# Kernel tuning notes

Hardware: AMD Instinct MI355X
Metric: run time of the kernel (lower is better)

The kernel has to match this reference:

```python
import jax, jax.numpy as jnp
import numpy as np

N_NODES = 50000
BN_EPS = 1e-5


def setup_inputs() -> dict:
    key = jax.random.key(0)
    ks = jax.random.split(key, 6)
    N, E, CIN, CH, COUT = N_NODES, 800000, 128, 256, 128
    node_feat = jax.random.normal(ks[0], (N, CIN), dtype=jnp.float32)
    edge_index = jax.random.randint(ks[1], (2, E), 0, N, dtype=jnp.int64)
    # Glorot-ish init for weights
    W1 = jax.random.normal(ks[2], (CIN, CH), dtype=jnp.float32) / np.sqrt(CIN)
    b1 = jnp.zeros((CH,), dtype=jnp.float32)
    bn_gamma = jnp.ones((CH,), dtype=jnp.float32)
    bn_beta = jnp.zeros((CH,), dtype=jnp.float32)
    W2 = jax.random.normal(ks[3], (CH, COUT), dtype=jnp.float32) / np.sqrt(CH)
    b2 = jnp.zeros((COUT,), dtype=jnp.float32)
    return {"node_feat": node_feat, "edge_index": edge_index, "W1": W1, "b1": b1,
            "bn_gamma": bn_gamma, "bn_beta": bn_beta, "W2": W2, "b2": b2}


def gcn_conv(x, W, b, src, dst, n_nodes):
    """PyG GCNConv: out = D^-1/2 (A+I) D^-1/2 (x W) + b."""
    h = x @ W                                   # [N, C_out]
    loop = jnp.arange(n_nodes, dtype=src.dtype)
    src_f = jnp.concatenate([src, loop])        # self-loops appended
    dst_f = jnp.concatenate([dst, loop])
    deg = jax.ops.segment_sum(jnp.ones_like(dst_f, dtype=h.dtype), dst_f,
                              num_segments=n_nodes)
    dinv = jax.lax.rsqrt(jnp.maximum(deg, 1.0))  # deg >= 1 due to self-loops
    norm = dinv[src_f] * dinv[dst_f]             # [E+N]
    msg = h[src_f] * norm[:, None]               # gather + scale
    return jax.ops.segment_sum(msg, dst_f, num_segments=n_nodes) + b


def batch_norm(x, gamma, beta):
    mean = jnp.mean(x, axis=0)
    var = jnp.mean((x - mean) ** 2, axis=0)      # biased var (torch BN normalization)
    return (x - mean) * jax.lax.rsqrt(var + BN_EPS) * gamma + beta


def reference(node_feat, edge_index, W1, b1, bn_gamma, bn_beta, W2, b2):
    src, dst = edge_index[0], edge_index[1]
    x = gcn_conv(node_feat, W1, b1, src, dst, N_NODES)
    x = batch_norm(x, bn_gamma, bn_beta)
    x = jax.nn.relu(x)
    # dropout is identity at inference
    x = gcn_conv(x, W2, b2, src, dst, N_NODES)
    return x
```

## Files before the change

kernel.cpp:

```cpp
#include <hip/hip_runtime.h>

#define CIN 128
#define CH 256
#define COUT 128
#define BN_EPS 1e-5f

typedef __attribute__((ext_vector_type(8))) short bf16x8;
typedef __attribute__((ext_vector_type(4))) float f32x4;

__device__ __forceinline__ short f2bf(float x) {
    unsigned u = __float_as_uint(x);
    unsigned r = (u + 0x7fffu + ((u >> 16) & 1u)) >> 16;
    return (short)r;
}
__device__ __forceinline__ float bf2f(short h) {
    return __uint_as_float(((unsigned)(unsigned short)h) << 16);
}

__device__ __forceinline__ void gather_edges(const short* __restrict__ xb,
                                             const unsigned short* __restrict__ csr,
                                             const float* __restrict__ dinv,
                                             int e0, int e1, float di, int c,
                                             float* acc) {
    int e = e0;
    for (; e + 7 < e1; e += 8) {
        int s[8];
        #pragma unroll
        for (int i = 0; i < 8; ++i) s[i] = csr[e + i];
        float w[8];
        #pragma unroll
        for (int i = 0; i < 8; ++i) w[i] = dinv[s[i]] * di;
        bf16x8 x[8];
        #pragma unroll
        for (int i = 0; i < 8; ++i) x[i] = *(const bf16x8*)(xb + (size_t)s[i] * 128 + c * 8);
        #pragma unroll
        for (int i = 0; i < 8; ++i)
            #pragma unroll
            for (int j = 0; j < 8; ++j) acc[j] = fmaf(w[i], bf2f(x[i][j]), acc[j]);
    }
    for (; e + 3 < e1; e += 4) {
        int s[4];
        #pragma unroll
        for (int i = 0; i < 4; ++i) s[i] = csr[e + i];
        float w[4];
        #pragma unroll
        for (int i = 0; i < 4; ++i) w[i] = dinv[s[i]] * di;
        bf16x8 x[4];
        #pragma unroll
        for (int i = 0; i < 4; ++i) x[i] = *(const bf16x8*)(xb + (size_t)s[i] * 128 + c * 8);
        #pragma unroll
        for (int i = 0; i < 4; ++i)
            #pragma unroll
            for (int j = 0; j < 8; ++j) acc[j] = fmaf(w[i], bf2f(x[i][j]), acc[j]);
    }
    for (; e < e1; ++e) {
        int s0 = csr[e];
        float ww = dinv[s0] * di;
        bf16x8 x0 = *(const bf16x8*)(xb + (size_t)s0 * 128 + c * 8);
        #pragma unroll
        for (int j = 0; j < 8; ++j) acc[j] = fmaf(ww, bf2f(x0[j]), acc[j]);
    }
}

__global__ void k_deg(const int* __restrict__ dst, int* __restrict__ degi,
                      unsigned short* __restrict__ rank, int E) {
    int e = blockIdx.x * 256 + threadIdx.x;
    if (e < E) rank[e] = (unsigned short)atomicAdd(&degi[dst[e]], 1);
}

__global__ void k_scan1(const int* __restrict__ degi, float* __restrict__ dinv,
                        int* __restrict__ blocksum, int* __restrict__ hist, int N) {
    __shared__ int s[256];
    __shared__ int h[256];
    int tid = threadIdx.x;
    h[tid] = 0;
    int i = blockIdx.x * 256 + tid;
    int v = (i < N) ? degi[i] : 0;
    if (i < N) dinv[i] = rsqrtf((float)(v + 1));
    s[tid] = v;
    __syncthreads();
    if (i < N) atomicAdd(&h[v > 255 ? 255 : v], 1);
    for (int st = 128; st > 0; st >>= 1) {
        if (tid < st) s[tid] += s[tid + st];
        __syncthreads();
    }
    if (tid == 0) blocksum[blockIdx.x] = s[0];
    int hv = h[tid];
    if (hv) atomicAdd(&hist[tid], hv);
}

__global__ void k_scan3(const int* __restrict__ degi, const int* __restrict__ blocksum,
                        int nb, int* __restrict__ rowstart,
                        const int* __restrict__ hist, int* __restrict__ histbase,
                        int N, int E) {
    __shared__ int sb[256];
    __shared__ int s[256];
    int tid = threadIdx.x;
    int bv = (tid < nb) ? blocksum[tid] : 0;
    sb[tid] = bv;
    __syncthreads();
    for (int st = 1; st < 256; st <<= 1) {
        int t = (tid >= st) ? sb[tid - st] : 0;
        __syncthreads();
        sb[tid] += t;
        __syncthreads();
    }
    int boff = (blockIdx.x == 0) ? 0 : sb[blockIdx.x - 1];

    int i = blockIdx.x * 256 + tid;
    int v = (i < N) ? degi[i] : 0;
    s[tid] = v;
    __syncthreads();
    for (int st = 1; st < 256; st <<= 1) {
        int t = (tid >= st) ? s[tid - st] : 0;
        __syncthreads();
        s[tid] += t;
        __syncthreads();
    }
    if (i < N) rowstart[i] = s[tid] - v + boff;
    if (blockIdx.x == 0 && tid == 0) rowstart[N] = E;

    if (blockIdx.x == 0) {
        __shared__ int hh[256];
        int own = hist[tid];
        hh[tid] = own;
        __syncthreads();
        for (int st = 1; st < 256; st <<= 1) {
            int t = (tid >= st) ? hh[tid - st] : 0;
            __syncthreads();
            hh[tid] += t;
            __syncthreads();
        }
        histbase[tid] = hh[tid] - own;
    }
}

__global__ void k_fillperm(const int* __restrict__ src, const int* __restrict__ dst,
                           const unsigned short* __restrict__ rank,
                           const int* __restrict__ rowstart,
                           unsigned short* __restrict__ csr,
                           const int* __restrict__ degi,
                           const int* __restrict__ histbase, int* __restrict__ histcnt,
                           int* __restrict__ perm, int E, int N, int nbE) {
    __shared__ int h[256];
    __shared__ int base[256];
    int tid = threadIdx.x;
    if ((int)blockIdx.x < nbE) {
        int e = blockIdx.x * 256 + tid;
        if (e < E) {
            int d = dst[e];
            int pos = rowstart[d] + (int)rank[e];
            __builtin_nontemporal_store((unsigned short)src[e], &csr[pos]);
        }
        return;
    }
    int i0 = ((int)blockIdx.x - nbE) * 1024;
    h[tid] = 0;
    __syncthreads();
    int d[4], lr[4];
    #pragma unroll
    for (int k = 0; k < 4; ++k) {
        int i = i0 + k * 256 + tid;
        if (i < N) {
            int dd = degi[i];
            if (dd > 255) dd = 255;
            d[k] = dd;
            lr[k] = atomicAdd(&h[dd], 1);
        } else {
            d[k] = -1;
        }
    }
    __syncthreads();
    int cnt = h[tid];
    if (cnt > 0) base[tid] = atomicAdd(&histcnt[tid], cnt);
    __syncthreads();
    #pragma unroll
    for (int k = 0; k < 4; ++k) {
        if (d[k] >= 0)
            perm[histbase[d[k]] + base[d[k]] + lr[k]] = i0 + k * 256 + tid;
    }
}

__global__ void k_prep(const float* __restrict__ W1, const float* __restrict__ W2,
                       short* __restrict__ W1sw, short* __restrict__ W2sw,
                       const float4* __restrict__ nf, short4* __restrict__ nfb,
                       int* __restrict__ degi, float* __restrict__ stats,
                       int* __restrict__ hist, int n4, int N) {
    int t = blockIdx.x * 256 + threadIdx.x;
    if (t < 32768) {
        if (t < 512) stats[t] = 0.0f;
        else if (t < 1024) hist[t - 512] = 0;
        int n = t >> 7, kk = t & 127;
        float v = W1[kk * 256 + n];
        int t16 = n >> 4, m = n & 15;
        int ks = kk >> 5, q = (kk >> 3) & 3, j = kk & 7;
        W1sw[(t16 * 4 + ks) * 512 + (q * 16 + m) * 8 + j] = f2bf(v);
    } else if (t < 65536) {
        int u = t - 32768;
        int n = u >> 8, kk = u & 255;
        float v = W2[kk * 128 + n];
        int t16 = n >> 4, m = n & 15;
        int ks = kk >> 5, q = (kk >> 3) & 3, j = kk & 7;
        W2sw[(t16 * 8 + ks) * 512 + (q * 16 + m) * 8 + j] = f2bf(v);
    } else {
        int u = t - 65536;
        if (u < n4) {
            float4 v = nf[u];
            short4 s;
            s.x = f2bf(v.x); s.y = f2bf(v.y); s.z = f2bf(v.z); s.w = f2bf(v.w);
            nfb[u] = s;
        } else {
            int u2 = u - n4;
            if (u2 < N) degi[u2] = 0;
        }
    }
}

__global__ __launch_bounds__(256, 4) void k_gemm1g(
        const short* __restrict__ xb, const int* __restrict__ rowstart,
        const unsigned short* __restrict__ csr, const float* __restrict__ dinv,
        const int* __restrict__ perm, const short* __restrict__ Bsw,
        const float* __restrict__ bias, short* __restrict__ C,
        float* __restrict__ stats, int M) {
    constexpr int K = CIN, NOUT = CH;
    constexpr int CT = NOUT / 64;
    constexpr int KS = K / 32;
    constexpr int KP = K + 8;
    constexpr int LROW = NOUT + 8;
    constexpr int LSZ = (64 * KP > 64 * LROW) ? 64 * KP : 64 * LROW;
    __shared__ __align__(16) short lds[LSZ];
    __shared__ int prow[64];
    int tid = threadIdx.x;
    int wave = tid >> 6;
    int lane = tid & 63;
    int m = lane & 15;
    int q = lane >> 4;
    int row0 = blockIdx.x * 64;
    if (tid < 64) {
        int pos = row0 + tid;
        if (pos >= M) pos = M - 1;
        prow[tid] = perm[M - 1 - pos];
    }
    __syncthreads();

    int c = tid & 15;
    int g = tid >> 4;
    #pragma unroll
    for (int p = 0; p < 4; ++p) {
        int rl = p * 16 + g;
        int r = prow[rl];
        float di = dinv[r];
        float w0 = di * di;
        bf16x8 sv = *(const bf16x8*)(xb + (size_t)r * 128 + c * 8);
        float acc[8];
        #pragma unroll
        for (int j = 0; j < 8; ++j) acc[j] = bf2f(sv[j]) * w0;
        gather_edges(xb, csr, dinv, rowstart[r], rowstart[r + 1], di, c, acc);
        bf16x8 h;
        #pragma unroll
        for (int j = 0; j < 8; ++j) h[j] = f2bf(acc[j]);
        *(bf16x8*)(lds + rl * KP + c * 8) = h;
    }
    __syncthreads();

    f32x4 acc4[4][CT];
    #pragma unroll
    for (int rt = 0; rt < 4; ++rt)
        #pragma unroll
        for (int ct = 0; ct < CT; ++ct)
            acc4[rt][ct] = (f32x4){0.f, 0.f, 0.f, 0.f};

    #pragma unroll
    for (int ks = 0; ks < KS; ++ks) {
        bf16x8 bh[CT];
        #pragma unroll
        for (int ct = 0; ct < CT; ++ct)
            bh[ct] = *(const bf16x8*)(Bsw + (size_t)((wave * CT + ct) * KS + ks) * 512 + lane * 8);
        bf16x8 af[4];
        #pragma unroll
        for (int rt = 0; rt < 4; ++rt)
            af[rt] = *(const bf16x8*)(lds + (rt * 16 + m) * KP + ks * 32 + q * 8);
        #pragma unroll
        for (int ct = 0; ct < CT; ++ct)
            #pragma unroll
            for (int rt = 0; rt < 4; ++rt)
                acc4[rt][ct] = __builtin_amdgcn_mfma_f32_16x16x32_bf16(af[rt], bh[ct], acc4[rt][ct], 0, 0, 0);
    }
    __syncthreads();

    #pragma unroll
    for (int ct = 0; ct < CT; ++ct) {
        int col = wave * (NOUT / 4) + ct * 16 + m;
        float bv = bias[col];
        float s = 0.f, sq = 0.f;
        #pragma unroll
        for (int rt = 0; rt < 4; ++rt) {
            #pragma unroll
            for (int r = 0; r < 4; ++r) {
                int lrow = rt * 16 + q * 4 + r;
                float v = acc4[rt][ct][r] + bv;
                if (row0 + lrow < M) { s += v; sq = fmaf(v, v, sq); }
                lds[lrow * LROW + col] = f2bf(v);
            }
        }
        s += __shfl_xor(s, 16, 64);
        s += __shfl_xor(s, 32, 64);
        sq += __shfl_xor(sq, 16, 64);
        sq += __shfl_xor(sq, 32, 64);
        if (lane < 16) {
            unsafeAtomicAdd(&stats[col], s);
            unsafeAtomicAdd(&stats[256 + col], sq);
        }
    }
    __syncthreads();
    constexpr int CPR = NOUT / 8;
    #pragma unroll
    for (int i = 0; i < (64 * CPR) / 256; ++i) {
        int idx = i * 256 + tid;
        int row = idx / CPR;
        int ch = idx % CPR;
        if (row0 + row < M)
            *(bf16x8*)(C + (size_t)prow[row] * NOUT + ch * 8) =
                *(const bf16x8*)(lds + row * LROW + ch * 8);
    }
}

__device__ __forceinline__ bf16x8 bnrelu8(bf16x8 raw, const float* __restrict__ scsh, int c) {
    float4 sc0 = *(const float4*)(scsh + c);
    float4 sc1 = *(const float4*)(scsh + c + 4);
    float4 sh0 = *(const float4*)(scsh + 256 + c);
    float4 sh1 = *(const float4*)(scsh + 256 + c + 4);
    bf16x8 o;
    o[0] = f2bf(fmaxf(fmaf(bf2f(raw[0]), sc0.x, sh0.x), 0.f));
    o[1] = f2bf(fmaxf(fmaf(bf2f(raw[1]), sc0.y, sh0.y), 0.f));
    o[2] = f2bf(fmaxf(fmaf(bf2f(raw[2]), sc0.z, sh0.z), 0.f));
    o[3] = f2bf(fmaxf(fmaf(bf2f(raw[3]), sc0.w, sh0.w), 0.f));
    o[4] = f2bf(fmaxf(fmaf(bf2f(raw[4]), sc1.x, sh1.x), 0.f));
    o[5] = f2bf(fmaxf(fmaf(bf2f(raw[5]), sc1.y, sh1.y), 0.f));
    o[6] = f2bf(fmaxf(fmaf(bf2f(raw[6]), sc1.z, sh1.z), 0.f));
    o[7] = f2bf(fmaxf(fmaf(bf2f(raw[7]), sc1.w, sh1.w), 0.f));
    return o;
}

__global__ __launch_bounds__(256, 4) void k_gemm2(
        const short* __restrict__ A, const short* __restrict__ Bsw,
        const float* __restrict__ stats, const float* __restrict__ gamma,
        const float* __restrict__ beta, short* __restrict__ C, int M) {
    constexpr int K = CH, NOUT = COUT;
    constexpr int CT = NOUT / 64;
    constexpr int KS = K / 32;
    constexpr int KP = K + 8;
    constexpr int LROW = NOUT + 8;
    constexpr int LSZ = (64 * KP > 64 * LROW) ? 64 * KP : 64 * LROW;
    __shared__ __align__(16) short lds[LSZ];
    __shared__ float scsh[512];
    int tid = threadIdx.x;
    int wave = tid >> 6;
    int lane = tid & 63;
    int m = lane & 15;
    int q = lane >> 4;
    int row0 = blockIdx.x * 64;

    if (tid < 256) {
        float invN = 1.0f / (float)M;
        float mean = stats[tid] * invN;
        float var = fmaxf(stats[256 + tid] * invN - mean * mean, 0.f);
        float inv = rsqrtf(var + BN_EPS);
        float sc = gamma[tid] * inv;
        scsh[tid] = sc;
        scsh[256 + tid] = fmaf(-mean, sc, beta[tid]);
    }
    __syncthreads();

    constexpr int CPRA = K / 8;
    #pragma unroll
    for (int i = 0; i < (64 * CPRA) / 256; ++i) {
        int idx = i * 256 + tid;
        int r = idx / CPRA, cc = idx % CPRA;
        int gr = row0 + r;
        if (gr >= M) gr = M - 1;
        bf16x8 v = *(const bf16x8*)(A + (size_t)gr * K + cc * 8);
        v = bnrelu8(v, scsh, cc * 8);
        *(bf16x8*)(lds + r * KP + cc * 8) = v;
    }
    __syncthreads();

    f32x4 acc[4][CT];
    #pragma unroll
    for (int rt = 0; rt < 4; ++rt)
        #pragma unroll
        for (int ct = 0; ct < CT; ++ct)
            acc[rt][ct] = (f32x4){0.f, 0.f, 0.f, 0.f};

    #pragma unroll
    for (int ks = 0; ks < KS; ++ks) {
        bf16x8 bh[CT];
        #pragma unroll
        for (int ct = 0; ct < CT; ++ct)
            bh[ct] = *(const bf16x8*)(Bsw + (size_t)((wave * CT + ct) * KS + ks) * 512 + lane * 8);
        bf16x8 af[4];
        #pragma unroll
        for (int rt = 0; rt < 4; ++rt)
            af[rt] = *(const bf16x8*)(lds + (rt * 16 + m) * KP + ks * 32 + q * 8);
        #pragma unroll
        for (int ct = 0; ct < CT; ++ct)
            #pragma unroll
            for (int rt = 0; rt < 4; ++rt)
                acc[rt][ct] = __builtin_amdgcn_mfma_f32_16x16x32_bf16(af[rt], bh[ct], acc[rt][ct], 0, 0, 0);
    }
    __syncthreads();

    #pragma unroll
    for (int ct = 0; ct < CT; ++ct) {
        int col = wave * (NOUT / 4) + ct * 16 + m;
        #pragma unroll
        for (int rt = 0; rt < 4; ++rt) {
            #pragma unroll
            for (int r = 0; r < 4; ++r) {
                int lrow = rt * 16 + q * 4 + r;
                lds[lrow * LROW + col] = f2bf(acc[rt][ct][r]);
            }
        }
    }
    __syncthreads();
    constexpr int CPR = NOUT / 8;
    #pragma unroll
    for (int i = 0; i < (64 * CPR) / 256; ++i) {
        int idx = i * 256 + tid;
        int row = idx / CPR;
        int ch = idx % CPR;
        if (row0 + row < M)
            *(bf16x8*)(C + (size_t)(row0 + row) * NOUT + ch * 8) =
                *(const bf16x8*)(lds + row * LROW + ch * 8);
    }
}

__global__ __launch_bounds__(256) void k_gather1(
        const short* __restrict__ yb, const int* __restrict__ rowstart,
        const unsigned short* __restrict__ csr, const float* __restrict__ dinv,
        const int* __restrict__ perm, const float* __restrict__ bias,
        float* __restrict__ out, int N) {
    int t = blockIdx.x * 256 + threadIdx.x;
    int sp = t >> 4;
    int c = t & 15;
    if (sp >= N) return;
    int r = perm[N - 1 - sp];
    float di = dinv[r];
    float w0 = di * di;
    bf16x8 sv = *(const bf16x8*)(yb + (size_t)r * 128 + c * 8);
    float acc[8];
    #pragma unroll
    for (int j = 0; j < 8; ++j) acc[j] = bf2f(sv[j]) * w0;
    gather_edges(yb, csr, dinv, rowstart[r], rowstart[r + 1], di, c, acc);
    float4 b0 = *(const float4*)(bias + c * 8);
    float4 b1 = *(const float4*)(bias + c * 8 + 4);
    float4 o0 = make_float4(acc[0] + b0.x, acc[1] + b0.y, acc[2] + b0.z, acc[3] + b0.w);
    float4 o1 = make_float4(acc[4] + b1.x, acc[5] + b1.y, acc[6] + b1.z, acc[7] + b1.w);
    *(float4*)(out + (size_t)r * 128 + c * 8) = o0;
    *(float4*)(out + (size_t)r * 128 + c * 8 + 4) = o1;
}

extern "C" void kernel_launch(void* const* d_in, const int* in_sizes, int n_in,
                              void* d_out, int out_size, void* d_ws, size_t ws_size,
                              hipStream_t stream) {
    const float* nf    = (const float*)d_in[0];
    const int*   ei    = (const int*)d_in[1];
    const float* W1    = (const float*)d_in[2];
    const float* b1    = (const float*)d_in[3];
    const float* gamma = (const float*)d_in[4];
    const float* beta  = (const float*)d_in[5];
    const float* W2    = (const float*)d_in[6];
    const float* b2    = (const float*)d_in[7];
    float* out = (float*)d_out;

    const int N = in_sizes[0] / CIN;
    const int E = in_sizes[1] / 2;
    const int* src = ei;
    const int* dst = ei + E;

    const int nb1 = (N + 63) / 64;

    char* ws = (char*)d_ws;
    auto align256 = [](size_t x) { return (x + 255) & ~(size_t)255; };
    size_t off = 0;
    int*   degi = (int*)(ws + off);      off += align256((size_t)N * 4);
    float* stats = (float*)(ws + off);   off += align256(512 * 4);
    float* dinv = (float*)(ws + off);    off += align256((size_t)N * 4);
    int*   rowstart = (int*)(ws + off);  off += align256((size_t)(N + 1) * 4);
    int*   blocksum = (int*)(ws + off);  off += align256(256 * 4);
    int*   hist = (int*)(ws + off);      off += align256(512 * 4);
    int*   histbase = (int*)(ws + off);  off += align256(256 * 4);
    int*   perm = (int*)(ws + off);      off += align256((size_t)N * 4);
    short* W1sw = (short*)(ws + off);    off += align256(32768 * 2);
    short* W2sw = (short*)(ws + off);    off += align256(32768 * 2);
    unsigned short* rank = (unsigned short*)(ws + off); off += align256((size_t)E * 2);
    unsigned short* csr = (unsigned short*)(ws + off);  off += align256((size_t)E * 2);
    short* nfb = (short*)(ws + off);     off += align256((size_t)N * CIN * 2);
    short* x1b = (short*)(ws + off);     off += align256((size_t)N * CH * 2);
    short* yb = (short*)(ws + off);      off += align256((size_t)N * COUT * 2);

    int nbN = (N + 255) / 256;
    int nbE = (E + 255) / 256;
    int nbP = (N + 1023) / 1024;
    int n4 = N * 32;

    k_prep<<<(65536 + n4 + N + 255) / 256, 256, 0, stream>>>(
        W1, W2, W1sw, W2sw, (const float4*)nf, (short4*)nfb, degi, stats, hist, n4, N);

    k_deg<<<nbE, 256, 0, stream>>>(dst, degi, rank, E);
    k_scan1<<<nbN, 256, 0, stream>>>(degi, dinv, blocksum, hist, N);
    k_scan3<<<nbN, 256, 0, stream>>>(degi, blocksum, nbN, rowstart, hist, histbase, N, E);
    k_fillperm<<<nbE + nbP, 256, 0, stream>>>(
        src, dst, rank, rowstart, csr, degi, histbase, hist + 256, perm, E, N, nbE);

    k_gemm1g<<<nb1, 256, 0, stream>>>(nfb, rowstart, csr, dinv, perm, W1sw, b1, x1b, stats, N);

    k_gemm2<<<nb1, 256, 0, stream>>>(x1b, W2sw, stats, gamma, beta, yb, N);

    k_gather1<<<(N * 16 + 255) / 256, 256, 0, stream>>>(
        yb, rowstart, csr, dinv, perm, b2, out, N);
}
```

Measured before the change: 251.1 us.

## Precompute edge weights into CSR and widen gemm1 blocks to 512 threads

The CSR entries grow from a 16-bit source index to a (weight, source) pair, with the normalization dinv[s]*dinv[d] computed once during CSR fill. Both gather passes then skip the dependent dinv lookup. Separately, the fused gather+GEMM1 kernel runs with 512 threads, so each wave covers 32 output columns and each thread gathers two rows instead of four, for more parallelism in the gather phase. In exchange, the CSR array is four times larger, which adds fill-time writes and gather-time reads, and the nontemporal store is dropped.

```diff
diff --git a/kernel.cpp b/kernel.cpp
--- a/kernel.cpp
+++ b/kernel.cpp
@@ -18,47 +18,44 @@
 }
 
 __device__ __forceinline__ void gather_edges(const short* __restrict__ xb,
-                                             const unsigned short* __restrict__ csr,
-                                             const float* __restrict__ dinv,
-                                             int e0, int e1, float di, int c,
+                                             const uint2* __restrict__ csr,
+                                             int e0, int e1, int c,
                                              float* acc) {
     int e = e0;
     for (; e + 7 < e1; e += 8) {
-        int s[8];
-        #pragma unroll
-        for (int i = 0; i < 8; ++i) s[i] = csr[e + i];
-        float w[8];
-        #pragma unroll
-        for (int i = 0; i < 8; ++i) w[i] = dinv[s[i]] * di;
+        uint2 ew[8];
+        #pragma unroll
+        for (int i = 0; i < 8; ++i) ew[i] = csr[e + i];
         bf16x8 x[8];
         #pragma unroll
-        for (int i = 0; i < 8; ++i) x[i] = *(const bf16x8*)(xb + (size_t)s[i] * 128 + c * 8);
-        #pragma unroll
-        for (int i = 0; i < 8; ++i)
+        for (int i = 0; i < 8; ++i) x[i] = *(const bf16x8*)(xb + (size_t)ew[i].y * 128 + c * 8);
+        #pragma unroll
+        for (int i = 0; i < 8; ++i) {
+            float w = __uint_as_float(ew[i].x);
             #pragma unroll
-            for (int j = 0; j < 8; ++j) acc[j] = fmaf(w[i], bf2f(x[i][j]), acc[j]);
+            for (int j = 0; j < 8; ++j) acc[j] = fmaf(w, bf2f(x[i][j]), acc[j]);
+        }
     }
     for (; e + 3 < e1; e += 4) {
-        int s[4];
-        #pragma unroll
-        for (int i = 0; i < 4; ++i) s[i] = csr[e + i];
-        float w[4];
-        #pragma unroll
-        for (int i = 0; i < 4; ++i) w[i] = dinv[s[i]] * di;
+        uint2 ew[4];
+        #pragma unroll
+        for (int i = 0; i < 4; ++i) ew[i] = csr[e + i];
         bf16x8 x[4];
         #pragma unroll
-        for (int i = 0; i < 4; ++i) x[i] = *(const bf16x8*)(xb + (size_t)s[i] * 128 + c * 8);
-        #pragma unroll
-        for (int i = 0; i < 4; ++i)
+        for (int i = 0; i < 4; ++i) x[i] = *(const bf16x8*)(xb + (size_t)ew[i].y * 128 + c * 8);
+        #pragma unroll
+        for (int i = 0; i < 4; ++i) {
+            float w = __uint_as_float(ew[i].x);
             #pragma unroll
-            for (int j = 0; j < 8; ++j) acc[j] = fmaf(w[i], bf2f(x[i][j]), acc[j]);
+            for (int j = 0; j < 8; ++j) acc[j] = fmaf(w, bf2f(x[i][j]), acc[j]);
+        }
     }
     for (; e < e1; ++e) {
-        int s0 = csr[e];
-        float ww = dinv[s0] * di;
-        bf16x8 x0 = *(const bf16x8*)(xb + (size_t)s0 * 128 + c * 8);
-        #pragma unroll
-        for (int j = 0; j < 8; ++j) acc[j] = fmaf(ww, bf2f(x0[j]), acc[j]);
+        uint2 ew = csr[e];
+        float w = __uint_as_float(ew.x);
+        bf16x8 x0 = *(const bf16x8*)(xb + (size_t)ew.y * 128 + c * 8);
+        #pragma unroll
+        for (int j = 0; j < 8; ++j) acc[j] = fmaf(w, bf2f(x0[j]), acc[j]);
     }
 }
 
@@ -138,7 +135,8 @@
 __global__ void k_fillperm(const int* __restrict__ src, const int* __restrict__ dst,
                            const unsigned short* __restrict__ rank,
                            const int* __restrict__ rowstart,
-                           unsigned short* __restrict__ csr,
+                           const float* __restrict__ dinv,
+                           uint2* __restrict__ csr,
                            const int* __restrict__ degi,
                            const int* __restrict__ histbase, int* __restrict__ histcnt,
                            int* __restrict__ perm, int E, int N, int nbE) {
@@ -149,8 +147,12 @@
         int e = blockIdx.x * 256 + tid;
         if (e < E) {
             int d = dst[e];
+            int s = src[e];
             int pos = rowstart[d] + (int)rank[e];
-            __builtin_nontemporal_store((unsigned short)src[e], &csr[pos]);
+            uint2 ev;
+            ev.x = __float_as_uint(dinv[s] * dinv[d]);
+            ev.y = (unsigned)s;
+            csr[pos] = ev;
         }
         return;
     }
@@ -216,14 +218,14 @@
     }
 }
 
-__global__ __launch_bounds__(256, 4) void k_gemm1g(
+__global__ __launch_bounds__(512, 4) void k_gemm1g(
         const short* __restrict__ xb, const int* __restrict__ rowstart,
-        const unsigned short* __restrict__ csr, const float* __restrict__ dinv,
+        const uint2* __restrict__ csr, const float* __restrict__ dinv,
         const int* __restrict__ perm, const short* __restrict__ Bsw,
         const float* __restrict__ bias, short* __restrict__ C,
         float* __restrict__ stats, int M) {
     constexpr int K = CIN, NOUT = CH;
-    constexpr int CT = NOUT / 64;
+    constexpr int CT = NOUT / 128;
     constexpr int KS = K / 32;
     constexpr int KP = K + 8;
     constexpr int LROW = NOUT + 8;
@@ -246,8 +248,8 @@
     int c = tid & 15;
     int g = tid >> 4;
     #pragma unroll
-    for (int p = 0; p < 4; ++p) {
-        int rl = p * 16 + g;
+    for (int p = 0; p < 2; ++p) {
+        int rl = p * 32 + g;
         int r = prow[rl];
         float di = dinv[r];
         float w0 = di * di;
@@ -255,7 +257,7 @@
         float acc[8];
         #pragma unroll
         for (int j = 0; j < 8; ++j) acc[j] = bf2f(sv[j]) * w0;
-        gather_edges(xb, csr, dinv, rowstart[r], rowstart[r + 1], di, c, acc);
+        gather_edges(xb, csr, rowstart[r], rowstart[r + 1], c, acc);
         bf16x8 h;
         #pragma unroll
         for (int j = 0; j < 8; ++j) h[j] = f2bf(acc[j]);
@@ -290,7 +292,7 @@
 
     #pragma unroll
     for (int ct = 0; ct < CT; ++ct) {
-        int col = wave * (NOUT / 4) + ct * 16 + m;
+        int col = wave * 32 + ct * 16 + m;
         float bv = bias[col];
         float s = 0.f, sq = 0.f;
         #pragma unroll
@@ -315,8 +317,8 @@
     __syncthreads();
     constexpr int CPR = NOUT / 8;
     #pragma unroll
-    for (int i = 0; i < (64 * CPR) / 256; ++i) {
-        int idx = i * 256 + tid;
+    for (int i = 0; i < (64 * CPR) / 512; ++i) {
+        int idx = i * 512 + tid;
         int row = idx / CPR;
         int ch = idx % CPR;
         if (row0 + row < M)
@@ -437,7 +439,7 @@
 
 __global__ __launch_bounds__(256) void k_gather1(
         const short* __restrict__ yb, const int* __restrict__ rowstart,
-        const unsigned short* __restrict__ csr, const float* __restrict__ dinv,
+        const uint2* __restrict__ csr, const float* __restrict__ dinv,
         const int* __restrict__ perm, const float* __restrict__ bias,
         float* __restrict__ out, int N) {
     int t = blockIdx.x * 256 + threadIdx.x;
@@ -451,7 +453,7 @@
     float acc[8];
     #pragma unroll
     for (int j = 0; j < 8; ++j) acc[j] = bf2f(sv[j]) * w0;
-    gather_edges(yb, csr, dinv, rowstart[r], rowstart[r + 1], di, c, acc);
+    gather_edges(yb, csr, rowstart[r], rowstart[r + 1], c, acc);
     float4 b0 = *(const float4*)(bias + c * 8);
     float4 b1 = *(const float4*)(bias + c * 8 + 4);
     float4 o0 = make_float4(acc[0] + b0.x, acc[1] + b0.y, acc[2] + b0.z, acc[3] + b0.w);
@@ -494,7 +496,7 @@
     short* W1sw = (short*)(ws + off);    off += align256(32768 * 2);
     short* W2sw = (short*)(ws + off);    off += align256(32768 * 2);
     unsigned short* rank = (unsigned short*)(ws + off); off += align256((size_t)E * 2);
-    unsigned short* csr = (unsigned short*)(ws + off);  off += align256((size_t)E * 2);
+    uint2* csr = (uint2*)(ws + off);     off += align256((size_t)E * 8);
     short* nfb = (short*)(ws + off);     off += align256((size_t)N * CIN * 2);
     short* x1b = (short*)(ws + off);     off += align256((size_t)N * CH * 2);
     short* yb = (short*)(ws + off);      off += align256((size_t)N * COUT * 2);
@@ -511,9 +513,9 @@
     k_scan1<<<nbN, 256, 0, stream>>>(degi, dinv, blocksum, hist, N);
     k_scan3<<<nbN, 256, 0, stream>>>(degi, blocksum, nbN, rowstart, hist, histbase, N, E);
     k_fillperm<<<nbE + nbP, 256, 0, stream>>>(
-        src, dst, rank, rowstart, csr, degi, histbase, hist + 256, perm, E, N, nbE);
-
-    k_gemm1g<<<nb1, 256, 0, stream>>>(nfb, rowstart, csr, dinv, perm, W1sw, b1, x1b, stats, N);
+        src, dst, rank, rowstart, dinv, csr, degi, histbase, hist + 256, perm, E, N, nbE);
+
+    k_gemm1g<<<nb1, 512, 0, stream>>>(nfb, rowstart, csr, dinv, perm, W1sw, b1, x1b, stats, N);
 
     k_gemm2<<<nb1, 256, 0, stream>>>(x1b, W2sw, stats, gamma, beta, yb, N);
 
```

Result: faster. 242.4 us (-3.5%).
